# Kernel optimization log

Hardware: AMD Instinct MI355X
Metric: run time of the kernel (lower is better)

Reference implementation:

```python
import jax, jax.numpy as jnp
import numpy as np
from jax import lax

TRAJ_STEPS = 50  # output_dim=100 -> 50 (x,y) waypoints


def setup_inputs() -> dict:
    key = jax.random.key(0)
    ks = jax.random.split(key, 12)
    s = 0.05  # small init scale to keep gates out of saturation
    return {
        "x": jax.random.normal(ks[0], (32768, 256), jnp.float32),
        "W1": jax.random.normal(ks[1], (256, 64), jnp.float32) * s,
        "b1": jax.random.normal(ks[2], (64,), jnp.float32) * s,
        "W2": jax.random.normal(ks[3], (64, 64), jnp.float32) * s,
        "b2": jax.random.normal(ks[4], (64,), jnp.float32) * s,
        "Wih": jax.random.normal(ks[5], (2, 192), jnp.float32) * s,   # GRU input weights, gate order (r,z,n)
        "bih": jax.random.normal(ks[6], (192,), jnp.float32) * s,
        "Whh": jax.random.normal(ks[7], (64, 192), jnp.float32) * s,  # GRU hidden weights
        "bhh": jax.random.normal(ks[8], (192,), jnp.float32) * s,
        "Wout": jax.random.normal(ks[9], (64, 2), jnp.float32) * s,
        "bout": jax.random.normal(ks[10], (2,), jnp.float32) * s,
    }


def _forward(x, W1, b1, W2, b2, Wih, bih, Whh, bhh, Wout, bout):
    H = W2.shape[1]
    # backbone MLP -> initial hidden state
    z = jax.nn.relu(x @ W1 + b1)
    z = jax.nn.relu(z @ W2 + b2)  # [B, H]

    def step(carry, _):
        wp, h = carry                      # wp: [B,2] current waypoint, h: [B,H]
        gi = wp @ Wih + bih                # [B, 3H]
        gh = h @ Whh + bhh                 # [B, 3H]
        ir, iz, inn = gi[..., :H], gi[..., H:2 * H], gi[..., 2 * H:]
        hr, hz, hn = gh[..., :H], gh[..., H:2 * H], gh[..., 2 * H:]
        r = jax.nn.sigmoid(ir + hr)
        u = jax.nn.sigmoid(iz + hz)
        n = jnp.tanh(inn + r * hn)
        h_new = (1.0 - u) * n + u * h      # PyTorch GRUCell update
        dx = jax.nn.sigmoid(h_new @ Wout + bout)  # [B,2]
        wp_new = wp + dx                   # residual accumulation
        return (wp_new, h_new), wp_new

    wp0 = jnp.zeros(x.shape[:-1] + (2,), z.dtype)
    _, wps = lax.scan(step, (wp0, z), None, length=TRAJ_STEPS)  # [T, B, 2]
    wps = jnp.moveaxis(wps, 0, -2)                              # [B, T, 2]
    return wps.reshape(x.shape[:-1] + (2 * TRAJ_STEPS,))        # [B, 2T]


def reference(x, W1, b1, W2, b2, Wih, bih, Whh, bhh, Wout, bout):
    return _forward(x, W1, b1, W2, b2, Wih, bih, Whh, bhh, Wout, bout)
```

## Files before the change

### kernel.cpp

```cpp
#include <hip/hip_runtime.h>
#include <hip/hip_bf16.h>

#define TRAJ 50

typedef __attribute__((ext_vector_type(8))) short short8;
typedef __attribute__((ext_vector_type(4))) float f32x4;

#if defined(__has_builtin)
#if __has_builtin(__builtin_amdgcn_exp2f)
#define EXP2F(x) __builtin_amdgcn_exp2f(x)
#else
#define EXP2F(x) exp2f(x)
#endif
#if __has_builtin(__builtin_amdgcn_rcpf)
#define RCPF(x) __builtin_amdgcn_rcpf(x)
#else
#define RCPF(x) (1.0f/(x))
#endif
#else
#define EXP2F(x) exp2f(x)
#define RCPF(x) (1.0f/(x))
#endif

__device__ __forceinline__ unsigned short f2bf(float f){
  union { float f; unsigned u; } v; v.f = f;
  unsigned u = v.u;
  u += 0x7FFFu + ((u >> 16) & 1u);
  return (unsigned short)(u >> 16);
}
__device__ __forceinline__ unsigned pk(unsigned short a, unsigned short b){
  return (unsigned)a | ((unsigned)b << 16);
}
__device__ __forceinline__ unsigned pkbf(float a, float b){
  union { __hip_bfloat162 h; unsigned u; } c;
  c.h = __float22bfloat162_rn(make_float2(a, b));
  return c.u;
}
__device__ __forceinline__ short8 mkfrag(uint2 v){
  union { unsigned u[4]; short8 s; } c;
  c.u[0] = v.x; c.u[1] = v.y; c.u[2] = 0u; c.u[3] = 0u;
  return c.s;
}

#define MFMA16(A,B,C) __builtin_amdgcn_mfma_f32_16x16x32_bf16((A),(B),(C),0,0,0)

#define SSC (-1.44269504f)
#define TSC ( 2.88539008f)

__global__ __launch_bounds__(512, 4) void gru_actor_kernel(
    const float* __restrict__ x,
    const float* __restrict__ W1, const float* __restrict__ b1,
    const float* __restrict__ W2, const float* __restrict__ b2,
    const float* __restrict__ Wih, const float* __restrict__ bih,
    const float* __restrict__ Whh, const float* __restrict__ bhh,
    const float* __restrict__ Wout, const float* __restrict__ bout,
    float* __restrict__ out)
{
  __shared__ __align__(16) char sm_x[32768];
  __shared__ __align__(16) char sm_w[32768];
  __shared__ __align__(16) char sm_w2[8192];
  __shared__ __align__(16) char sm_wo[2048];
  __shared__ float sm_b1[64];
  __shared__ float sm_b2[64];

  const int t    = threadIdx.x;
  const int row0 = blockIdx.x * 64;
  const int w    = t >> 6;
  const int pair = w >> 1;
  const int p    = w & 1;
  const int l    = t & 63;
  const int lr   = l & 15;
  const int lg   = l >> 4;
  const int myrow = pair * 16 + lr;
  const int swz  = (lr & 7) << 4;

  {
    const float4* xg = (const float4*)(x + (size_t)row0 * 256);
    #pragma unroll
    for (int it = 0; it < 8; ++it){
      int fi = t + it * 512;
      float4 v = xg[fi];
      int e = fi * 4, row = e >> 8, col = e & 255;
      *(uint2*)(sm_x + row * 512 + ((col * 2) ^ ((row & 7) << 4))) =
          make_uint2(pkbf(v.x, v.y), pkbf(v.z, v.w));
    }
  }
  for (int n = t; n < 16384; n += 512){
    int i = n & 63, kk = n >> 6;
    *(unsigned short*)(sm_w + i * 512 + ((kk * 2) ^ ((i & 7) << 4))) = f2bf(W1[kk * 64 + i]);
  }
  for (int n = t; n < 4096; n += 512){
    int i = n & 63, kk = n >> 6;
    *(unsigned short*)(sm_w2 + i * 128 + ((kk * 2) ^ ((i & 7) << 4))) = f2bf(W2[kk * 64 + i]);
  }
  for (int n = t; n < 1024; n += 512){
    int row = n & 15, k = n >> 4;
    float v = (row < 2) ? SSC * Wout[k * 2 + row] : 0.0f;
    *(unsigned short*)(sm_wo + row * 128 + k * 2) = f2bf(v);
  }
  if (t < 64){ sm_b1[t] = b1[t]; sm_b2[t] = b2[t]; }
  __syncthreads();

  const int ar0 = 16 * (2 * p + 0) + lr;
  const int ar1 = 16 * (2 * p + 1) + lr;
  f32x4 accL0, accL1;
  {
    float4 bva = *(const float4*)(sm_b1 + 16 * (2 * p + 0) + lg * 4);
    float4 bvb = *(const float4*)(sm_b1 + 16 * (2 * p + 1) + lg * 4);
    accL0 = (f32x4){bva.x, bva.y, bva.z, bva.w};
    accL1 = (f32x4){bvb.x, bvb.y, bvb.z, bvb.w};
  }
  #pragma unroll
  for (int kb = 0; kb < 8; ++kb){
    short8 B  = *(const short8*)(sm_x + myrow * 512 + ((kb * 64 + lg * 16) ^ swz));
    short8 Aa = *(const short8*)(sm_w + ar0 * 512 + ((kb * 64 + lg * 16) ^ swz));
    short8 Ab = *(const short8*)(sm_w + ar1 * 512 + ((kb * 64 + lg * 16) ^ swz));
    accL0 = MFMA16(Aa, B, accL0);
    accL1 = MFMA16(Ab, B, accL1);
  }
  __syncthreads();

  {
    f32x4 a0 = accL0, a1 = accL1;
    *(uint2*)(sm_x + myrow * 128 + ((64 * p + 0  + 8 * lg) ^ swz)) =
        make_uint2(pkbf(fmaxf(a0[0],0.f), fmaxf(a0[1],0.f)), pkbf(fmaxf(a0[2],0.f), fmaxf(a0[3],0.f)));
    *(uint2*)(sm_x + myrow * 128 + ((64 * p + 32 + 8 * lg) ^ swz)) =
        make_uint2(pkbf(fmaxf(a1[0],0.f), fmaxf(a1[1],0.f)), pkbf(fmaxf(a1[2],0.f), fmaxf(a1[3],0.f)));
  }
  for (int n = t; n < 12288; n += 512){
    int kk = n / 192, i = n - kk * 192;
    float s = (i < 128) ? SSC : TSC;
    *(unsigned short*)(sm_w + i * 128 + ((kk * 2) ^ ((i & 7) << 4))) = f2bf(s * Whh[kk * 192 + i]);
  }
  __syncthreads();

  float h[8];
  {
    f32x4 acc20, acc21;
    float4 bva = *(const float4*)(sm_b2 + 16 * (2 * p + 0) + lg * 4);
    float4 bvb = *(const float4*)(sm_b2 + 16 * (2 * p + 1) + lg * 4);
    acc20 = (f32x4){bva.x, bva.y, bva.z, bva.w};
    acc21 = (f32x4){bvb.x, bvb.y, bvb.z, bvb.w};
    #pragma unroll
    for (int kb = 0; kb < 2; ++kb){
      short8 B  = *(const short8*)(sm_x + myrow * 128 + ((kb * 64 + lg * 16) ^ swz));
      short8 Aa = *(const short8*)(sm_w2 + ar0 * 128 + ((kb * 64 + lg * 16) ^ swz));
      short8 Ab = *(const short8*)(sm_w2 + ar1 * 128 + ((kb * 64 + lg * 16) ^ swz));
      acc20 = MFMA16(Aa, B, acc20);
      acc21 = MFMA16(Ab, B, acc21);
    }
    #pragma unroll
    for (int r = 0; r < 4; ++r){ h[r] = fmaxf(acc20[r], 0.f); h[4 + r] = fmaxf(acc21[r], 0.f); }
    *(uint2*)(sm_x + 8192 + myrow * 128 + ((64 * p + 0  + 8 * lg) ^ swz)) =
        make_uint2(pkbf(h[0], h[1]), pkbf(h[2], h[3]));
    *(uint2*)(sm_x + 8192 + myrow * 128 + ((64 * p + 32 + 8 * lg) ^ swz)) =
        make_uint2(pkbf(h[4], h[5]), pkbf(h[6], h[7]));
  }

  short8 Ah[3][2][2];
  #pragma unroll
  for (int g = 0; g < 3; ++g){
    #pragma unroll
    for (int tql = 0; tql < 2; ++tql){
      int i = g * 64 + 32 * p + 16 * tql + lr;
      #pragma unroll
      for (int kb = 0; kb < 2; ++kb)
        Ah[g][tql][kb] = *(const short8*)(sm_w + i * 128 + ((kb * 64 + lg * 16) ^ swz));
    }
  }
  uint2 Ak2p[4][2] = {};
  if (lg == 0){
    #pragma unroll
    for (int tql = 0; tql < 2; ++tql){
      int dr = 32 * p + 16 * tql + lr;
      int du = 64 + dr, dn = 128 + dr;
      Ak2p[0][tql] = make_uint2(pk(f2bf(SSC*Wih[dr]), f2bf(SSC*Wih[192+dr])),
                                pk(f2bf(SSC*(bih[dr]+bhh[dr])), 0));
      Ak2p[1][tql] = make_uint2(pk(f2bf(SSC*Wih[du]), f2bf(SSC*Wih[192+du])),
                                pk(f2bf(SSC*(bih[du]+bhh[du])), 0));
      Ak2p[2][tql] = make_uint2(0u, pk(f2bf(TSC*bhh[dn]), 0));
      Ak2p[3][tql] = make_uint2(pk(f2bf(TSC*Wih[dn]), f2bf(TSC*Wih[192+dn])),
                                pk(f2bf(TSC*bih[dn]), 0));
    }
  }
  const float bo0 = SSC * bout[0], bo1 = SSC * bout[1];
  __syncthreads();

  float wp0 = 0.f, wp1 = 0.f;
  float* outp = out + (size_t)(row0 + myrow) * 100;
  short8 B0 = *(const short8*)(sm_x + 8192 + myrow * 128 + ((0  + lg * 16) ^ swz));
  short8 B1 = *(const short8*)(sm_x + 8192 + myrow * 128 + ((64 + lg * 16) ^ swz));

  #pragma unroll 1
  for (int s = 0; s < TRAJ; ++s){
    char* bufW = sm_x + ((s & 1) << 13);
    short8 B2;
    {
      unsigned b2lo = 0u, b2hi = 0u;
      if (lg == 0){ b2lo = pkbf(wp0, wp1); b2hi = 0x00003F80u; }
      union { unsigned u[4]; short8 sv; } c;
      c.u[0] = b2lo; c.u[1] = b2hi; c.u[2] = 0u; c.u[3] = 0u;
      B2 = c.sv;
    }
    #pragma unroll
    for (int tql = 0; tql < 2; ++tql){
      f32x4 aR = (f32x4){0,0,0,0}, aU = (f32x4){0,0,0,0};
      f32x4 aN = (f32x4){0,0,0,0}, aI = (f32x4){0,0,0,0};
      aR = MFMA16(Ah[0][tql][0], B0, aR);
      aR = MFMA16(Ah[0][tql][1], B1, aR);
      aR = MFMA16(mkfrag(Ak2p[0][tql]), B2, aR);
      aU = MFMA16(Ah[1][tql][0], B0, aU);
      aU = MFMA16(Ah[1][tql][1], B1, aU);
      aU = MFMA16(mkfrag(Ak2p[1][tql]), B2, aU);
      aN = MFMA16(Ah[2][tql][0], B0, aN);
      aN = MFMA16(Ah[2][tql][1], B1, aN);
      aN = MFMA16(mkfrag(Ak2p[2][tql]), B2, aN);
      aI = MFMA16(mkfrag(Ak2p[3][tql]), B2, aI);
      #pragma unroll
      for (int r = 0; r < 4; ++r){
        float e1 = EXP2F(aR[r]);
        float e2 = EXP2F(aU[r]);
        float d1 = 1.f + e1, d2 = 1.f + e2;
        float rp = RCPF(d1 * d2);
        float rv = d2 * rp;
        float uv = d1 * rp;
        float y  = fmaf(rv, aN[r], aI[r]);
        float nv = fmaf(-2.f, RCPF(1.f + EXP2F(y)), 1.f);
        int hi_ = 4 * tql + r;
        h[hi_] = fmaf(uv, h[hi_] - nv, nv);
      }
      *(uint2*)(bufW + myrow * 128 + ((64 * p + 32 * tql + 8 * lg) ^ swz)) =
          make_uint2(pkbf(h[4*tql+0], h[4*tql+1]), pkbf(h[4*tql+2], h[4*tql+3]));
    }
    __syncthreads();
    short8 nB0 = *(const short8*)(bufW + myrow * 128 + ((0  + lg * 16) ^ swz));
    short8 nB1 = *(const short8*)(bufW + myrow * 128 + ((64 + lg * 16) ^ swz));
    short8 Ao0 = *(const short8*)(sm_wo + lr * 128 + 0  + lg * 16);
    short8 Ao1 = *(const short8*)(sm_wo + lr * 128 + 64 + lg * 16);
    f32x4 aD = (f32x4){0,0,0,0};
    if (lg == 0){ aD[0] = bo0; aD[1] = bo1; }
    aD = MFMA16(Ao0, nB0, aD);
    aD = MFMA16(Ao1, nB1, aD);
    if (lg == 0){
      float ea = EXP2F(aD[0]), eb = EXP2F(aD[1]);
      float da = 1.f + ea, db = 1.f + eb;
      float rp = RCPF(da * db);
      wp0 += db * rp;
      wp1 += da * rp;
      if (p == 0) *(float2*)(outp + 2 * s) = make_float2(wp0, wp1);
    }
    B0 = nB0; B1 = nB1;
  }
}

extern "C" void kernel_launch(void* const* d_in, const int* in_sizes, int n_in,
                              void* d_out, int out_size, void* d_ws, size_t ws_size,
                              hipStream_t stream) {
  (void)n_in; (void)out_size; (void)d_ws; (void)ws_size;
  const float* x    = (const float*)d_in[0];
  const float* W1   = (const float*)d_in[1];
  const float* b1   = (const float*)d_in[2];
  const float* W2   = (const float*)d_in[3];
  const float* b2   = (const float*)d_in[4];
  const float* Wih  = (const float*)d_in[5];
  const float* bih  = (const float*)d_in[6];
  const float* Whh  = (const float*)d_in[7];
  const float* bhh  = (const float*)d_in[8];
  const float* Wout = (const float*)d_in[9];
  const float* bout = (const float*)d_in[10];
  float* out = (float*)d_out;

  int nrows = in_sizes[0] / 256;
  int grid  = nrows / 64;
  gru_actor_kernel<<<dim3(grid), dim3(512), 0, stream>>>(
      x, W1, b1, W2, b2, Wih, bih, Whh, bhh, Wout, bout, out);
}
```

Baseline: 117.7 us.

## Stage waypoints in LDS, keep Wout fragments in registers, pack GRU math

Each step's waypoint output is written to LDS as packed bf16 instead of as a scattered global float2 store. The whole 64x100 tile is then written to global memory once, with coalesced stores, after the recurrence. The Wout MFMA fragments are built in registers once rather than reloaded from LDS every step. The gate math is rewritten on float2 vectors so the compiler can use packed FP32 instructions, and the step loop is unrolled by two. Storing waypoints as bf16 truncates the accumulated output values, which risks accuracy failures.

```diff
diff --git a/kernel.cpp b/kernel.cpp
--- a/kernel.cpp
+++ b/kernel.cpp
@@ -5,6 +5,7 @@
 
 typedef __attribute__((ext_vector_type(8))) short short8;
 typedef __attribute__((ext_vector_type(4))) float f32x4;
+typedef __attribute__((ext_vector_type(2))) float f32x2;
 
 #if defined(__has_builtin)
 #if __has_builtin(__builtin_amdgcn_exp2f)
@@ -47,6 +48,21 @@
 #define SSC (-1.44269504f)
 #define TSC ( 2.88539008f)
 
+__device__ __forceinline__ f32x2 exp2v(f32x2 v){ return (f32x2){EXP2F(v[0]), EXP2F(v[1])}; }
+__device__ __forceinline__ f32x2 rcpv (f32x2 v){ return (f32x2){RCPF(v[0]), RCPF(v[1])}; }
+
+__device__ __forceinline__ f32x2 gru_pair(f32x2 r_, f32x2 u_, f32x2 n_, f32x2 i_, f32x2 hp){
+  const f32x2 one = (f32x2){1.f, 1.f};
+  f32x2 d1 = exp2v(r_) + one;
+  f32x2 d2 = exp2v(u_) + one;
+  f32x2 rp = rcpv(d1 * d2);
+  f32x2 rv = d2 * rp;
+  f32x2 uv = d1 * rp;
+  f32x2 y  = __builtin_elementwise_fma(rv, n_, i_);
+  f32x2 nv = one - 2.f * rcpv(exp2v(y) + one);
+  return __builtin_elementwise_fma(uv, hp - nv, nv);
+}
+
 __global__ __launch_bounds__(512, 4) void gru_actor_kernel(
     const float* __restrict__ x,
     const float* __restrict__ W1, const float* __restrict__ b1,
@@ -59,7 +75,6 @@
   __shared__ __align__(16) char sm_x[32768];
   __shared__ __align__(16) char sm_w[32768];
   __shared__ __align__(16) char sm_w2[8192];
-  __shared__ __align__(16) char sm_wo[2048];
   __shared__ float sm_b1[64];
   __shared__ float sm_b2[64];
 
@@ -93,11 +108,6 @@
     int i = n & 63, kk = n >> 6;
     *(unsigned short*)(sm_w2 + i * 128 + ((kk * 2) ^ ((i & 7) << 4))) = f2bf(W2[kk * 64 + i]);
   }
-  for (int n = t; n < 1024; n += 512){
-    int row = n & 15, k = n >> 4;
-    float v = (row < 2) ? SSC * Wout[k * 2 + row] : 0.0f;
-    *(unsigned short*)(sm_wo + row * 128 + k * 2) = f2bf(v);
-  }
   if (t < 64){ sm_b1[t] = b1[t]; sm_b2[t] = b2[t]; }
   __syncthreads();
 
@@ -134,7 +144,7 @@
   }
   __syncthreads();
 
-  float h[8];
+  f32x2 h2[4];
   {
     f32x4 acc20, acc21;
     float4 bva = *(const float4*)(sm_b2 + 16 * (2 * p + 0) + lg * 4);
@@ -149,12 +159,14 @@
       acc20 = MFMA16(Aa, B, acc20);
       acc21 = MFMA16(Ab, B, acc21);
     }
-    #pragma unroll
-    for (int r = 0; r < 4; ++r){ h[r] = fmaxf(acc20[r], 0.f); h[4 + r] = fmaxf(acc21[r], 0.f); }
+    h2[0] = (f32x2){fmaxf(acc20[0],0.f), fmaxf(acc20[1],0.f)};
+    h2[1] = (f32x2){fmaxf(acc20[2],0.f), fmaxf(acc20[3],0.f)};
+    h2[2] = (f32x2){fmaxf(acc21[0],0.f), fmaxf(acc21[1],0.f)};
+    h2[3] = (f32x2){fmaxf(acc21[2],0.f), fmaxf(acc21[3],0.f)};
     *(uint2*)(sm_x + 8192 + myrow * 128 + ((64 * p + 0  + 8 * lg) ^ swz)) =
-        make_uint2(pkbf(h[0], h[1]), pkbf(h[2], h[3]));
+        make_uint2(pkbf(h2[0][0], h2[0][1]), pkbf(h2[1][0], h2[1][1]));
     *(uint2*)(sm_x + 8192 + myrow * 128 + ((64 * p + 32 + 8 * lg) ^ swz)) =
-        make_uint2(pkbf(h[4], h[5]), pkbf(h[6], h[7]));
+        make_uint2(pkbf(h2[2][0], h2[2][1]), pkbf(h2[3][0], h2[3][1]));
   }
 
   short8 Ah[3][2][2];
@@ -183,15 +195,27 @@
                                 pk(f2bf(TSC*bih[dn]), 0));
     }
   }
+  short8 AoR[2];
+  #pragma unroll
+  for (int kb = 0; kb < 2; ++kb){
+    short8 f = (short8){0,0,0,0,0,0,0,0};
+    if (lr < 2){
+      #pragma unroll
+      for (int j = 0; j < 8; ++j){
+        int k = kb * 32 + lg * 8 + j;
+        f[j] = (short)f2bf(SSC * Wout[k * 2 + lr]);
+      }
+    }
+    AoR[kb] = f;
+  }
   const float bo0 = SSC * bout[0], bo1 = SSC * bout[1];
   __syncthreads();
 
   float wp0 = 0.f, wp1 = 0.f;
-  float* outp = out + (size_t)(row0 + myrow) * 100;
   short8 B0 = *(const short8*)(sm_x + 8192 + myrow * 128 + ((0  + lg * 16) ^ swz));
   short8 B1 = *(const short8*)(sm_x + 8192 + myrow * 128 + ((64 + lg * 16) ^ swz));
 
-  #pragma unroll 1
+  #pragma unroll 2
   for (int s = 0; s < TRAJ; ++s){
     char* bufW = sm_x + ((s & 1) << 13);
     short8 B2;
@@ -216,40 +240,40 @@
       aN = MFMA16(Ah[2][tql][1], B1, aN);
       aN = MFMA16(mkfrag(Ak2p[2][tql]), B2, aN);
       aI = MFMA16(mkfrag(Ak2p[3][tql]), B2, aI);
-      #pragma unroll
-      for (int r = 0; r < 4; ++r){
-        float e1 = EXP2F(aR[r]);
-        float e2 = EXP2F(aU[r]);
-        float d1 = 1.f + e1, d2 = 1.f + e2;
-        float rp = RCPF(d1 * d2);
-        float rv = d2 * rp;
-        float uv = d1 * rp;
-        float y  = fmaf(rv, aN[r], aI[r]);
-        float nv = fmaf(-2.f, RCPF(1.f + EXP2F(y)), 1.f);
-        int hi_ = 4 * tql + r;
-        h[hi_] = fmaf(uv, h[hi_] - nv, nv);
-      }
+      f32x2 hA = gru_pair((f32x2){aR[0],aR[1]}, (f32x2){aU[0],aU[1]},
+                          (f32x2){aN[0],aN[1]}, (f32x2){aI[0],aI[1]}, h2[2*tql+0]);
+      f32x2 hB = gru_pair((f32x2){aR[2],aR[3]}, (f32x2){aU[2],aU[3]},
+                          (f32x2){aN[2],aN[3]}, (f32x2){aI[2],aI[3]}, h2[2*tql+1]);
+      h2[2*tql+0] = hA; h2[2*tql+1] = hB;
       *(uint2*)(bufW + myrow * 128 + ((64 * p + 32 * tql + 8 * lg) ^ swz)) =
-          make_uint2(pkbf(h[4*tql+0], h[4*tql+1]), pkbf(h[4*tql+2], h[4*tql+3]));
+          make_uint2(pkbf(hA[0], hA[1]), pkbf(hB[0], hB[1]));
     }
     __syncthreads();
     short8 nB0 = *(const short8*)(bufW + myrow * 128 + ((0  + lg * 16) ^ swz));
     short8 nB1 = *(const short8*)(bufW + myrow * 128 + ((64 + lg * 16) ^ swz));
-    short8 Ao0 = *(const short8*)(sm_wo + lr * 128 + 0  + lg * 16);
-    short8 Ao1 = *(const short8*)(sm_wo + lr * 128 + 64 + lg * 16);
     f32x4 aD = (f32x4){0,0,0,0};
     if (lg == 0){ aD[0] = bo0; aD[1] = bo1; }
-    aD = MFMA16(Ao0, nB0, aD);
-    aD = MFMA16(Ao1, nB1, aD);
+    aD = MFMA16(AoR[0], nB0, aD);
+    aD = MFMA16(AoR[1], nB1, aD);
     if (lg == 0){
       float ea = EXP2F(aD[0]), eb = EXP2F(aD[1]);
       float da = 1.f + ea, db = 1.f + eb;
       float rp = RCPF(da * db);
       wp0 += db * rp;
       wp1 += da * rp;
-      if (p == 0) *(float2*)(outp + 2 * s) = make_float2(wp0, wp1);
+      if (p == 0)
+        *(unsigned*)(sm_x + 16384 + myrow * 200 + s * 4) = pkbf(wp0, wp1);
     }
     B0 = nB0; B1 = nB1;
+  }
+
+  __syncthreads();
+  for (int n = t; n < 3200; n += 512){
+    int row = n / 50, s = n - row * 50;
+    unsigned u = *(const unsigned*)(sm_x + 16384 + row * 200 + s * 4);
+    union { unsigned u; float f; } a, b;
+    a.u = u << 16; b.u = u & 0xFFFF0000u;
+    *(float2*)(out + (size_t)(row0 + row) * 100 + 2 * s) = make_float2(a.f, b.f);
   }
 }
 
```

Result: slower. 128.0 us (+8.8%).
